# Kernel tuning notes

Hardware: AMD Instinct MI355X
Metric: run time of the kernel (lower is better)

The kernel has to match this reference:

```python
import jax, jax.numpy as jnp
import numpy as np

# --- quantization helpers (I-BERT-style symmetric quantization) ---

def _quant_int(x, scale, bit):
    # round(x/scale) clamped to signed `bit`-bit range (SymmetricQuantFunction)
    n = 2 ** (bit - 1) - 1
    return jnp.clip(jnp.round(x / scale), -n - 1, n)


def quant_linear(x, s_x, W, b, weight_bit=8):
    """QuantLinear: per-output-channel symmetric 8-bit weight quant, int GEMM, dequant.
    Returns (output, bias_scaling_factor[out_features])."""
    n = 2 ** (weight_bit - 1) - 1
    w_scale = jnp.maximum(jnp.max(jnp.abs(W), axis=1), 1e-8) / n          # (out,)
    w_int = _quant_int(W, w_scale[:, None], weight_bit)                   # int-valued (out,in)
    b_scale = w_scale * s_x                                               # (out,) broadcasts with scalar s_x
    b_int = jnp.round(b / b_scale)                                        # 32-bit bias, no clamp needed
    x_int = x / s_x                                                       # int-valued activations
    out_int = jnp.einsum('bsi,oi->bso', x_int, w_int) + b_int
    return out_int * b_scale, b_scale


def quant_act(x, bit):
    """QuantAct: per-tensor symmetric requantization to `bit` bits (dynamic min/max)."""
    n = 2 ** (bit - 1) - 1
    scale = jnp.maximum(jnp.max(jnp.abs(x)), 1e-8) / n                    # scalar
    x_int = _quant_int(x, scale, bit)
    return x_int * scale, scale


def int_gelu(x, s):
    """IntGELU (I-BERT): integer 2nd-order polynomial approximation of erf."""
    k = 1.4142
    c0, c1 = -0.2888, -1.769
    c2 = 1.0 / c0
    SHIFT = 14  # 'const' in the original code

    x_int = x / s
    se = s / k  # scaling factor fed to int_erf
    # --- int_erf ---
    b_int = jnp.floor(c1 / se)
    c_int = jnp.floor(c2 / se ** 2)
    sign = jnp.sign(x_int)
    abs_int = jnp.minimum(jnp.abs(x_int), -b_int)
    y_int = sign * ((abs_int + b_int) ** 2 + c_int)
    se2 = se ** 2 * c0
    y_int = jnp.floor(y_int / 2 ** SHIFT)
    se2 = se2 * 2 ** SHIFT
    # --- gelu = x * (erf/2 + 1/2) in integer form ---
    shift_int = jnp.floor(1.0 / se2)
    out_int = x_int * (y_int + shift_int)
    s_out = s * se2 / 2
    return out_int * s_out, s_out


def setup_inputs() -> dict:
    key = jax.random.key(0)
    k_x, k_w1, k_b1, k_w2, k_b2 = jax.random.split(key, 5)
    B, S, D, H = 8, 1024, 768, 3072
    x = jax.random.normal(k_x, (B, S, D), dtype=jnp.float32)
    act_scaling_factor = jnp.full((1,), 0.02, dtype=jnp.float32)
    # pre-quantize x onto its input grid (x arrives already quantized in the real pipeline)
    x = jnp.round(x / act_scaling_factor) * act_scaling_factor
    W1 = jax.random.normal(k_w1, (H, D), dtype=jnp.float32) * 0.02
    b1 = jax.random.normal(k_b1, (H,), dtype=jnp.float32) * 0.02
    W2 = jax.random.normal(k_w2, (D, H), dtype=jnp.float32) * 0.02
    b2 = jax.random.normal(k_b2, (D,), dtype=jnp.float32) * 0.02
    return {"x": x, "act_scaling_factor": act_scaling_factor,
            "W1": W1, "b1": b1, "W2": W2, "b2": b2}


def reference(x, act_scaling_factor, W1, b1, W2, b2):
    s = act_scaling_factor
    h, s = quant_linear(x, s, W1, b1)       # fc1: int8 GEMM + dequant
    h, s = quant_act(h, 8)                  # qact_gelu
    h, s = int_gelu(h, s)                   # IntGELU
    h, s = quant_act(h, 8)                  # qact1 (drop=0.0 -> identity)
    h, s = quant_linear(h, s, W2, b2)       # fc2
    h, s = quant_act(h, 16)                 # qact2 (16-bit)
    return h, s
```

## Files before the change

kernel.cpp:

```cpp
#include <hip/hip_runtime.h>

typedef _Float16 half8  __attribute__((ext_vector_type(8)));
typedef _Float16 half4v __attribute__((ext_vector_type(4)));
typedef float f32x4 __attribute__((ext_vector_type(4)));
typedef int int4v __attribute__((ext_vector_type(4)));

#define M_DIM 8192
#define D_DIM 768
#define H_DIM 3072

#define WS_WSCALE2   16
#define WS_BINT1     (WS_WSCALE2 + 768*4)
#define WS_BSCALE1   (WS_BINT1 + 3072*4)
#define WS_XQ        34560UL
#define WS_WQ1       (WS_XQ  + (size_t)M_DIM*D_DIM*2)
#define WS_WQ2I      (WS_WQ1 + (size_t)H_DIM*D_DIM*2)
#define WS_H1        (WS_WQ2I + (size_t)D_DIM*H_DIM)
#define WS_Q2        WS_H1
#define WS_H2        (WS_H1 + (size_t)M_DIM*H_DIM)
#define WS_Q1        (WS_H1 + (size_t)M_DIM*H_DIM*4)

__device__ __forceinline__ void gl_lds16(const _Float16* g, _Float16* l) {
  __builtin_amdgcn_global_load_lds(
      (const __attribute__((address_space(1))) void*)g,
      (__attribute__((address_space(3))) void*)l, 16, 0, 0);
}
__device__ __forceinline__ void gl_lds16c(const char* g, char* l) {
  __builtin_amdgcn_global_load_lds(
      (const __attribute__((address_space(1))) void*)g,
      (__attribute__((address_space(3))) void*)l, 16, 0, 0);
}
__device__ __forceinline__ void vmw4or0(bool four) {
  if (four) asm volatile("s_waitcnt vmcnt(4)" ::: "memory");
  else      asm volatile("s_waitcnt vmcnt(0)" ::: "memory");
}

struct GeluP { float scale1, bintg, cintg, shiftint, s_out; };

__device__ __forceinline__ GeluP gelu_params(float max1) {
  GeluP p;
  p.scale1 = fmaxf(max1, 1e-8f) / 127.0f;
  float se = p.scale1 / 1.4142f;
  p.bintg = floorf(-1.769f / se);
  p.cintg = floorf(((float)(1.0 / -0.2888)) / (se * se));
  float se2 = ((se * se) * -0.2888f) * 16384.0f;
  p.shiftint = floorf(1.0f / se2);
  p.s_out = (p.scale1 * se2) * 0.5f;
  return p;
}

__device__ __forceinline__ float gelu_val(const GeluP& p, float qf) {
  float sg = (qf > 0.f) ? 1.f : ((qf < 0.f) ? -1.f : 0.f);
  float aq = fminf(fabsf(qf), -p.bintg);
  float t = aq + p.bintg;
  float y = sg * (t * t + p.cintg);
  float yf = floorf(y * (1.0f / 16384.0f));
  return (qf * (yf + p.shiftint)) * p.s_out;
}

__global__ __launch_bounds__(256)
void k12_prep(const float* __restrict__ W1, const float* __restrict__ b1,
              const float* __restrict__ W2, const float* __restrict__ x,
              const float* __restrict__ sxp,
              _Float16* __restrict__ wq1, char* __restrict__ wq2i,
              float* __restrict__ wscale2, float* __restrict__ bint1,
              float* __restrict__ bscale1, _Float16* __restrict__ xq,
              unsigned* __restrict__ wsu)
{
  if (blockIdx.x == 0 && threadIdx.x == 0) { wsu[0] = 0u; wsu[1] = 0u; wsu[2] = 0u; }
  if (blockIdx.x < 960) {
    int w = blockIdx.x * 4 + (threadIdx.x >> 6);
    int lane = threadIdx.x & 63;
    if (w < H_DIM) {
      const float* row = W1 + (size_t)w * D_DIM;
      f32x4 v[3]; float m = 0.f;
#pragma unroll
      for (int t = 0; t < 3; t++) {
        v[t] = *(const f32x4*)(row + t * 256 + lane * 4);
#pragma unroll
        for (int j = 0; j < 4; j++) m = fmaxf(m, fabsf(v[t][j]));
      }
#pragma unroll
      for (int off = 32; off >= 1; off >>= 1) m = fmaxf(m, __shfl_xor(m, off));
      float wsc = fmaxf(m, 1e-8f) / 127.0f;
      _Float16* orow = wq1 + (size_t)w * D_DIM;
#pragma unroll
      for (int t = 0; t < 3; t++) {
        half4v h;
#pragma unroll
        for (int j = 0; j < 4; j++) {
          float q = fminf(fmaxf(rintf(v[t][j] / wsc), -128.f), 127.f);
          h[j] = (_Float16)q;
        }
        *(half4v*)(orow + t * 256 + lane * 4) = h;
      }
      if (lane == 0) {
        float bs = wsc * sxp[0];
        bint1[w] = rintf(b1[w] / bs);
        bscale1[w] = bs;
      }
    } else {
      int o = w - H_DIM;
      const float* row = W2 + (size_t)o * H_DIM;
      f32x4 v[12]; float m = 0.f;
#pragma unroll
      for (int t = 0; t < 12; t++) {
        v[t] = *(const f32x4*)(row + t * 256 + lane * 4);
#pragma unroll
        for (int j = 0; j < 4; j++) m = fmaxf(m, fabsf(v[t][j]));
      }
#pragma unroll
      for (int off = 32; off >= 1; off >>= 1) m = fmaxf(m, __shfl_xor(m, off));
      float wsc = fmaxf(m, 1e-8f) / 127.0f;
      unsigned* orow = (unsigned*)(wq2i + (size_t)o * H_DIM);
#pragma unroll
      for (int t = 0; t < 12; t++) {
        unsigned pk = 0;
#pragma unroll
        for (int j = 0; j < 4; j++) {
          float q = fminf(fmaxf(rintf(v[t][j] / wsc), -128.f), 127.f);
          pk |= ((unsigned)(unsigned char)(char)(int)q) << (8 * j);
        }
        orow[t * 64 + lane] = pk;
      }
      if (lane == 0) wscale2[o] = wsc;
    }
  } else {
    float sx = sxp[0];
    const int n4 = (M_DIM * D_DIM) / 4;
    const int stride = 1024 * 256;
    for (int i = (blockIdx.x - 960) * 256 + threadIdx.x; i < n4; i += stride) {
      f32x4 v = ((const f32x4*)x)[i];
      half4v h;
#pragma unroll
      for (int j = 0; j < 4; j++) h[j] = (_Float16)(v[j] / sx);
      ((half4v*)xq)[i] = h;
    }
  }
}

#define STAGE_A8(buf, h, t) do {                                              \
    const _Float16* _s = pa + (size_t)(h) * 128 * K + (size_t)(t) * 64;       \
    _Float16* _d = lds + (buf) * 32768 + (h) * 8192 + w * 512;                \
    gl_lds16(_s, _d);                                                         \
    gl_lds16(_s + (size_t)64 * K, _d + 4096);                                 \
  } while (0)
#define STAGE_B8(buf, h, t) do {                                              \
    const _Float16* _s = pb + (size_t)(h) * 128 * K + (size_t)(t) * 64;       \
    _Float16* _d = lds + (buf) * 32768 + 16384 + (h) * 8192 + w * 512;        \
    gl_lds16(_s, _d);                                                         \
    gl_lds16(_s + (size_t)64 * K, _d + 4096);                                 \
  } while (0)
#define PHASE8(buf, qq, DOB, STMT, VMSTMT) do {                               \
    const char* _sb = (const char*)lds + (buf) * 65536;                       \
    half8 a00 = *(const half8*)(_sb + abase + (2*(qq)) * 2048 + c0);          \
    half8 a01 = *(const half8*)(_sb + abase + (2*(qq)) * 2048 + c1);          \
    half8 a10 = *(const half8*)(_sb + abase + (2*(qq)+1) * 2048 + c0);        \
    half8 a11 = *(const half8*)(_sb + abase + (2*(qq)+1) * 2048 + c1);        \
    if (DOB) {                                                                \
      _Pragma("unroll")                                                       \
      for (int nf = 0; nf < 4; nf++) {                                        \
        bfr[nf][0] = *(const half8*)(_sb + bbase + nf * 2048 + c0);           \
        bfr[nf][1] = *(const half8*)(_sb + bbase + nf * 2048 + c1);           \
      }                                                                       \
    }                                                                         \
    STMT;                                                                     \
    VMSTMT;                                                                   \
    asm volatile("s_barrier" ::: "memory");                                   \
    __builtin_amdgcn_s_setprio(1);                                            \
    _Pragma("unroll")                                                         \
    for (int nf = 0; nf < 4; nf++) {                                          \
      acc[2*(qq)][nf]   = __builtin_amdgcn_mfma_f32_16x16x32_f16(a00, bfr[nf][0], acc[2*(qq)][nf],   0, 0, 0); \
      acc[2*(qq)][nf]   = __builtin_amdgcn_mfma_f32_16x16x32_f16(a01, bfr[nf][1], acc[2*(qq)][nf],   0, 0, 0); \
      acc[2*(qq)+1][nf] = __builtin_amdgcn_mfma_f32_16x16x32_f16(a10, bfr[nf][0], acc[2*(qq)+1][nf], 0, 0, 0); \
      acc[2*(qq)+1][nf] = __builtin_amdgcn_mfma_f32_16x16x32_f16(a11, bfr[nf][1], acc[2*(qq)+1][nf], 0, 0, 0); \
    }                                                                         \
    __builtin_amdgcn_s_setprio(0);                                            \
    asm volatile("s_barrier" ::: "memory");                                   \
  } while (0)

__global__ __launch_bounds__(512, 2)
void gemm_f16_8p(const _Float16* __restrict__ A, const _Float16* __restrict__ B,
                 const float* __restrict__ bint, const float* __restrict__ bscale,
                 float* __restrict__ C, unsigned* __restrict__ maxw, int N, int K)
{
  __shared__ _Float16 lds[65536];
  __shared__ float wred[8];
  const int tid = threadIdx.x;
  const int w = tid >> 6;
  const int l = tid & 63;
  const int m0 = blockIdx.x * 256;
  const int n0 = blockIdx.y * 256;
  const int wm = w >> 2;
  const int wn = w & 3;

  const int srow = 8 * w + (l >> 3);
  const int swc  = (l & 7) ^ (l >> 3);
  const _Float16* pa = A + (size_t)(m0 + srow) * K + swc * 8;
  const _Float16* pb = B + (size_t)(n0 + srow) * K + swc * 8;

  const int c0 = (((l >> 4)) ^ (l & 7)) * 16;
  const int c1 = ((4 + (l >> 4)) ^ (l & 7)) * 16;
  const int abase = (wm * 128 + (l & 15)) * 128;
  const int bbase = 32768 + (wn * 64 + (l & 15)) * 128;

  f32x4 acc[8][4];
#pragma unroll
  for (int i = 0; i < 8; i++)
#pragma unroll
    for (int j = 0; j < 4; j++) acc[i][j] = (f32x4){0.f, 0.f, 0.f, 0.f};
  half8 bfr[4][2];

  const int nt = K >> 6;
  STAGE_B8(0, 0, 0); STAGE_B8(0, 1, 0);
  STAGE_A8(0, 0, 0); STAGE_A8(0, 1, 0);
  STAGE_B8(1, 0, 1); STAGE_B8(1, 1, 1);
  asm volatile("s_waitcnt vmcnt(4)" ::: "memory");
  asm volatile("s_barrier" ::: "memory");

  for (int i = 0; i < (nt >> 1); ++i) {
    const int t0 = 2 * i, t1 = 2 * i + 1;
    const bool g = (t0 + 2 < nt);
    PHASE8(0, 0, true,  STAGE_A8(1, 0, t1), );
    PHASE8(0, 1, false, STAGE_A8(1, 1, t1), );
    PHASE8(0, 2, false, if (g) STAGE_B8(0, 0, t0 + 2), );
    PHASE8(0, 3, false, if (g) STAGE_B8(0, 1, t0 + 2), vmw4or0(g));
    PHASE8(1, 0, true,  if (g) STAGE_A8(0, 0, t0 + 2), );
    PHASE8(1, 1, false, if (g) STAGE_A8(0, 1, t0 + 2), );
    PHASE8(1, 2, false, if (g) STAGE_B8(1, 0, t1 + 2), );
    PHASE8(1, 3, false, if (g) STAGE_B8(1, 1, t1 + 2),
           if (g) asm volatile("s_waitcnt vmcnt(4)" ::: "memory"));
  }

  float tmax = 0.f;
  const int orow0 = m0 + wm * 128 + (l >> 4) * 4;
  const int ocol0 = n0 + wn * 64 + (l & 15);
#pragma unroll
  for (int nf = 0; nf < 4; nf++) {
    const int col = ocol0 + nf * 16;
    const float bi = bint[col];
    const float bs = bscale[col];
#pragma unroll
    for (int mi = 0; mi < 8; mi++) {
#pragma unroll
      for (int e = 0; e < 4; e++) {
        const int rowm = orow0 + mi * 16 + e;
        float v = (acc[mi][nf][e] + bi) * bs;
        C[(size_t)rowm * N + col] = v;
        tmax = fmaxf(tmax, fabsf(v));
      }
    }
  }
#pragma unroll
  for (int off = 32; off >= 1; off >>= 1) tmax = fmaxf(tmax, __shfl_xor(tmax, off));
  if (l == 0) wred[w] = tmax;
  __syncthreads();
  if (tid == 0) {
    float bm = 0.f;
#pragma unroll
    for (int i = 0; i < 8; i++) bm = fmaxf(bm, wred[i]);
    atomicMax(maxw, __float_as_uint(bm));
  }
}

__global__ __launch_bounds__(256)
void k4_gelu(const float* __restrict__ h1, const unsigned* __restrict__ wsu,
             char* __restrict__ q1, unsigned* __restrict__ maxw, int n4)
{
  GeluP p = gelu_params(__uint_as_float(wsu[0]));
  float tmax = 0.f;
  int stride = gridDim.x * blockDim.x;
  for (int i = blockIdx.x * blockDim.x + threadIdx.x; i < n4; i += stride) {
    f32x4 h = ((const f32x4*)h1)[i];
    unsigned pack = 0;
#pragma unroll
    for (int j = 0; j < 4; j++) {
      float qf = fminf(fmaxf(rintf(h[j] / p.scale1), -128.f), 127.f);
      tmax = fmaxf(tmax, fabsf(gelu_val(p, qf)));
      pack |= ((unsigned)(unsigned char)(char)(int)qf) << (8 * j);
    }
    ((unsigned*)q1)[i] = pack;
  }
#pragma unroll
  for (int off = 32; off >= 1; off >>= 1) tmax = fmaxf(tmax, __shfl_xor(tmax, off));
  __shared__ float wred[4];
  int wid = threadIdx.x >> 6;
  if ((threadIdx.x & 63) == 0) wred[wid] = tmax;
  __syncthreads();
  if (threadIdx.x == 0) {
    float bm = fmaxf(fmaxf(wred[0], wred[1]), fmaxf(wred[2], wred[3]));
    atomicMax(maxw, __float_as_uint(bm));
  }
}

__global__ __launch_bounds__(256)
void k5_q2(const char* __restrict__ q1, const unsigned* __restrict__ wsu,
           char* __restrict__ q2, int n16)
{
  GeluP p = gelu_params(__uint_as_float(wsu[0]));
  float scale2 = fmaxf(__uint_as_float(wsu[1]), 1e-8f) / 127.0f;
  int stride = gridDim.x * blockDim.x;
  for (int i = blockIdx.x * blockDim.x + threadIdx.x; i < n16; i += stride) {
    uint4 pk = ((const uint4*)q1)[i];
    uint4 o;
    unsigned* pw[4] = {&o.x, &o.y, &o.z, &o.w};
    unsigned pr[4] = {pk.x, pk.y, pk.z, pk.w};
#pragma unroll
    for (int w = 0; w < 4; w++) {
      unsigned acc = 0;
#pragma unroll
      for (int j = 0; j < 4; j++) {
        float qf = (float)(int)(signed char)(pr[w] >> (8 * j));
        float g = gelu_val(p, qf);
        float q2f = fminf(fmaxf(rintf(g / scale2), -128.f), 127.f);
        acc |= ((unsigned)(unsigned char)(char)(int)q2f) << (8 * j);
      }
      *pw[w] = acc;
    }
    ((uint4*)q2)[i] = o;
  }
}

#define I8_SLOT 12288

__global__ __launch_bounds__(256)
void gemm_i8_dp(const char* __restrict__ A, const char* __restrict__ B,
                const unsigned* __restrict__ wsu, const float* __restrict__ wscale2,
                const float* __restrict__ b2, float* __restrict__ C,
                unsigned* __restrict__ maxw, int N, int K)
{
  __shared__ char lds[3 * I8_SLOT];
  __shared__ float wred[4];
  const int tid = threadIdx.x;
  const int wid = tid >> 6;
  const int lane = tid & 63;
  const int m0 = blockIdx.x * 64;
  const int n0 = blockIdx.y * 128;
  const int wm = wid >> 1;
  const int wn = wid & 1;
  const float scale2 = fmaxf(__uint_as_float(wsu[1]), 1e-8f) / 127.0f;

  const int sr = tid >> 2;
  const int sc = tid & 3;
  const int csw = sc ^ ((sr >> 1) & 3);
  const char* pa  = A + (size_t)(m0 + sr) * K + csw * 16;
  const char* pb0 = B + (size_t)(n0 + sr) * K + csw * 16;
  const char* pb1 = B + (size_t)(n0 + 64 + sr) * K + csw * 16;

#define STAGE_I(t, s) do {                                                   \
    char* const base = lds + (s) * I8_SLOT + wid * 1024;                     \
    gl_lds16c(pa  + (size_t)(t) * 64, base);                                 \
    gl_lds16c(pb0 + (size_t)(t) * 64, base + 4096);                          \
    gl_lds16c(pb1 + (size_t)(t) * 64, base + 8192);                          \
  } while (0)

  int aoff[2], boff[4];
  const int ks = lane >> 4;
#pragma unroll
  for (int f = 0; f < 2; f++) {
    int r = wm * 32 + f * 16 + (lane & 15);
    aoff[f] = r * 64 + ((ks ^ ((r >> 1) & 3)) * 16);
  }
#pragma unroll
  for (int f = 0; f < 4; f++) {
    int rn = wn * 64 + f * 16 + (lane & 15);
    boff[f] = 4096 + rn * 64 + ((ks ^ ((rn >> 1) & 3)) * 16);
  }

  int4v acc[2][4];
#pragma unroll
  for (int i = 0; i < 2; i++)
#pragma unroll
    for (int j = 0; j < 4; j++) acc[i][j] = (int4v){0, 0, 0, 0};

  const int nt = K / 64;
  STAGE_I(0, 0);
  STAGE_I(1, 1);
  for (int t = 0; t < nt; ++t) {
    const int s = t % 3;
    if (t + 1 < nt) asm volatile("s_waitcnt vmcnt(3)" ::: "memory");
    else            asm volatile("s_waitcnt vmcnt(0)" ::: "memory");
    asm volatile("s_barrier" ::: "memory");
    if (t + 2 < nt) STAGE_I(t + 2, (t + 2) % 3);
    const char* sb = lds + s * I8_SLOT;
    int4v a[2], b01[2], b23[2];
#pragma unroll
    for (int f = 0; f < 2; f++) a[f] = *(const int4v*)(sb + aoff[f]);
    b01[0] = *(const int4v*)(sb + boff[0]);
    b01[1] = *(const int4v*)(sb + boff[1]);
    __builtin_amdgcn_s_setprio(1);
#pragma unroll
    for (int i = 0; i < 2; i++)
#pragma unroll
      for (int j = 0; j < 2; j++)
        acc[i][j] = __builtin_amdgcn_mfma_i32_16x16x64_i8(a[i], b01[j], acc[i][j], 0, 0, 0);
    __builtin_amdgcn_s_setprio(0);
    b23[0] = *(const int4v*)(sb + boff[2]);
    b23[1] = *(const int4v*)(sb + boff[3]);
    __builtin_amdgcn_s_setprio(1);
#pragma unroll
    for (int i = 0; i < 2; i++)
#pragma unroll
      for (int j = 0; j < 2; j++)
        acc[i][j + 2] = __builtin_amdgcn_mfma_i32_16x16x64_i8(a[i], b23[j], acc[i][j + 2], 0, 0, 0);
    __builtin_amdgcn_s_setprio(0);
  }
#undef STAGE_I

  float tmax = 0.f;
  const int orow0 = m0 + wm * 32 + (lane >> 4) * 4;
  const int ocol0 = n0 + wn * 64 + (lane & 15);
#pragma unroll
  for (int j = 0; j < 4; j++) {
    const int col = ocol0 + j * 16;
    const float bs = wscale2[col] * scale2;
    const float bi = rintf(b2[col] / bs);
#pragma unroll
    for (int i = 0; i < 2; i++) {
#pragma unroll
      for (int e = 0; e < 4; e++) {
        const int rowm = orow0 + i * 16 + e;
        float v = ((float)acc[i][j][e] + bi) * bs;
        C[(size_t)rowm * N + col] = v;
        tmax = fmaxf(tmax, fabsf(v));
      }
    }
  }
#pragma unroll
  for (int off = 32; off >= 1; off >>= 1) tmax = fmaxf(tmax, __shfl_xor(tmax, off));
  if (lane == 0) wred[wid] = tmax;
  __syncthreads();
  if (tid == 0) {
    float bm = fmaxf(fmaxf(wred[0], wred[1]), fmaxf(wred[2], wred[3]));
    atomicMax(maxw, __float_as_uint(bm));
  }
}

__global__ __launch_bounds__(256)
void k7_final(const float* __restrict__ h2, const unsigned* __restrict__ wsu,
              float* __restrict__ out, int n4, int ntot)
{
  float scale16 = fmaxf(__uint_as_float(wsu[2]), 1e-8f) / 32767.0f;
  int stride = gridDim.x * blockDim.x;
  for (int i = blockIdx.x * blockDim.x + threadIdx.x; i < n4; i += stride) {
    f32x4 v = ((const f32x4*)h2)[i];
    f32x4 o;
#pragma unroll
    for (int j = 0; j < 4; j++) {
      float q = fminf(fmaxf(rintf(v[j] / scale16), -32768.f), 32767.f);
      o[j] = q * scale16;
    }
    ((f32x4*)out)[i] = o;
  }
  if (blockIdx.x == 0 && threadIdx.x == 0) out[ntot] = scale16;
}

extern "C" void kernel_launch(void* const* d_in, const int* in_sizes, int n_in,
                              void* d_out, int out_size, void* d_ws, size_t ws_size,
                              hipStream_t stream)
{
  (void)in_sizes; (void)n_in; (void)out_size; (void)ws_size;
  const float* x  = (const float*)d_in[0];
  const float* sx = (const float*)d_in[1];
  const float* W1 = (const float*)d_in[2];
  const float* b1 = (const float*)d_in[3];
  const float* W2 = (const float*)d_in[4];
  const float* b2 = (const float*)d_in[5];
  float* out = (float*)d_out;
  char* ws = (char*)d_ws;

  unsigned* wsu   = (unsigned*)ws;
  float* wscale2  = (float*)(ws + WS_WSCALE2);
  float* bint1    = (float*)(ws + WS_BINT1);
  float* bscale1  = (float*)(ws + WS_BSCALE1);
  _Float16* xq    = (_Float16*)(ws + WS_XQ);
  _Float16* wq1   = (_Float16*)(ws + WS_WQ1);
  char* wq2i      = (char*)(ws + WS_WQ2I);
  float* h1       = (float*)(ws + WS_H1);
  char* q2        = (char*)(ws + WS_Q2);
  float* h2       = (float*)(ws + WS_H2);
  char* q1        = (char*)(ws + WS_Q1);

  k12_prep<<<dim3(1984), dim3(256), 0, stream>>>(W1, b1, W2, x, sx, wq1, wq2i,
                                                 wscale2, bint1, bscale1, xq, wsu);
  gemm_f16_8p<<<dim3(32, 12), dim3(512), 0, stream>>>(xq, wq1, bint1, bscale1, h1, wsu + 0, H_DIM, D_DIM);
  k4_gelu<<<dim3(2048), dim3(256), 0, stream>>>(h1, wsu, q1, wsu + 1, (M_DIM * H_DIM) / 4);
  k5_q2<<<dim3(2048), dim3(256), 0, stream>>>(q1, wsu, q2, (M_DIM * H_DIM) / 16);
  gemm_i8_dp<<<dim3(128, 6), dim3(256), 0, stream>>>(q2, wq2i, wsu, wscale2, b2, h2, wsu + 2, D_DIM, H_DIM);
  k7_final<<<dim3(2048), dim3(256), 0, stream>>>(h2, wsu, out, (M_DIM * D_DIM) / 4, M_DIM * D_DIM);
}
```

Baseline: 187.0 us.

## Rewrite fc1 f16 GEMM as 128x256 tile with triple-buffered K=32 pipeline

Replaces the 512-thread 256x256-tile fc1 GEMM, which used an 8-phase ping-pong schedule, with a 256-thread 128x256-tile kernel. The new kernel uses a simple three-slot LDS ring over K steps of 32 and one barrier per step. Each wave computes all 128 rows against its own 64 columns, so the grid doubles to 768 blocks for better CU balance. In exchange there are more barriers per unit of K, more A-fragment LDS reads per wave, and less B reuse per block.

```diff
diff --git a/kernel.cpp b/kernel.cpp
--- a/kernel.cpp
+++ b/kernel.cpp
@@ -30,10 +30,6 @@
       (const __attribute__((address_space(1))) void*)g,
       (__attribute__((address_space(3))) void*)l, 16, 0, 0);
 }
-__device__ __forceinline__ void vmw4or0(bool four) {
-  if (four) asm volatile("s_waitcnt vmcnt(4)" ::: "memory");
-  else      asm volatile("s_waitcnt vmcnt(0)" ::: "memory");
-}
 
 struct GeluP { float scale1, bintg, cintg, shiftint, s_out; };
 
@@ -139,113 +135,89 @@
   }
 }
 
-#define STAGE_A8(buf, h, t) do {                                              \
-    const _Float16* _s = pa + (size_t)(h) * 128 * K + (size_t)(t) * 64;       \
-    _Float16* _d = lds + (buf) * 32768 + (h) * 8192 + w * 512;                \
-    gl_lds16(_s, _d);                                                         \
-    gl_lds16(_s + (size_t)64 * K, _d + 4096);                                 \
-  } while (0)
-#define STAGE_B8(buf, h, t) do {                                              \
-    const _Float16* _s = pb + (size_t)(h) * 128 * K + (size_t)(t) * 64;       \
-    _Float16* _d = lds + (buf) * 32768 + 16384 + (h) * 8192 + w * 512;        \
-    gl_lds16(_s, _d);                                                         \
-    gl_lds16(_s + (size_t)64 * K, _d + 4096);                                 \
-  } while (0)
-#define PHASE8(buf, qq, DOB, STMT, VMSTMT) do {                               \
-    const char* _sb = (const char*)lds + (buf) * 65536;                       \
-    half8 a00 = *(const half8*)(_sb + abase + (2*(qq)) * 2048 + c0);          \
-    half8 a01 = *(const half8*)(_sb + abase + (2*(qq)) * 2048 + c1);          \
-    half8 a10 = *(const half8*)(_sb + abase + (2*(qq)+1) * 2048 + c0);        \
-    half8 a11 = *(const half8*)(_sb + abase + (2*(qq)+1) * 2048 + c1);        \
-    if (DOB) {                                                                \
-      _Pragma("unroll")                                                       \
-      for (int nf = 0; nf < 4; nf++) {                                        \
-        bfr[nf][0] = *(const half8*)(_sb + bbase + nf * 2048 + c0);           \
-        bfr[nf][1] = *(const half8*)(_sb + bbase + nf * 2048 + c1);           \
-      }                                                                       \
-    }                                                                         \
-    STMT;                                                                     \
-    VMSTMT;                                                                   \
-    asm volatile("s_barrier" ::: "memory");                                   \
-    __builtin_amdgcn_s_setprio(1);                                            \
-    _Pragma("unroll")                                                         \
-    for (int nf = 0; nf < 4; nf++) {                                          \
-      acc[2*(qq)][nf]   = __builtin_amdgcn_mfma_f32_16x16x32_f16(a00, bfr[nf][0], acc[2*(qq)][nf],   0, 0, 0); \
-      acc[2*(qq)][nf]   = __builtin_amdgcn_mfma_f32_16x16x32_f16(a01, bfr[nf][1], acc[2*(qq)][nf],   0, 0, 0); \
-      acc[2*(qq)+1][nf] = __builtin_amdgcn_mfma_f32_16x16x32_f16(a10, bfr[nf][0], acc[2*(qq)+1][nf], 0, 0, 0); \
-      acc[2*(qq)+1][nf] = __builtin_amdgcn_mfma_f32_16x16x32_f16(a11, bfr[nf][1], acc[2*(qq)+1][nf], 0, 0, 0); \
-    }                                                                         \
-    __builtin_amdgcn_s_setprio(0);                                            \
-    asm volatile("s_barrier" ::: "memory");                                   \
-  } while (0)
-
-__global__ __launch_bounds__(512, 2)
-void gemm_f16_8p(const _Float16* __restrict__ A, const _Float16* __restrict__ B,
+__global__ __launch_bounds__(256, 2)
+void gemm_f16_v8(const _Float16* __restrict__ A, const _Float16* __restrict__ B,
                  const float* __restrict__ bint, const float* __restrict__ bscale,
                  float* __restrict__ C, unsigned* __restrict__ maxw, int N, int K)
 {
-  __shared__ _Float16 lds[65536];
-  __shared__ float wred[8];
+  __shared__ _Float16 lds[3 * 12288];
+  __shared__ float wred[4];
   const int tid = threadIdx.x;
   const int w = tid >> 6;
   const int l = tid & 63;
-  const int m0 = blockIdx.x * 256;
+  const int m0 = blockIdx.x * 128;
   const int n0 = blockIdx.y * 256;
-  const int wm = w >> 2;
-  const int wn = w & 3;
-
-  const int srow = 8 * w + (l >> 3);
-  const int swc  = (l & 7) ^ (l >> 3);
-  const _Float16* pa = A + (size_t)(m0 + srow) * K + swc * 8;
-  const _Float16* pb = B + (size_t)(n0 + srow) * K + swc * 8;
-
-  const int c0 = (((l >> 4)) ^ (l & 7)) * 16;
-  const int c1 = ((4 + (l >> 4)) ^ (l & 7)) * 16;
-  const int abase = (wm * 128 + (l & 15)) * 128;
-  const int bbase = 32768 + (wn * 64 + (l & 15)) * 128;
+
+  const int sri = l >> 2;
+  const int csw = (l & 3) ^ ((l >> 3) & 3);
+  const _Float16* pag = A + (size_t)(m0 + 32 * w + sri) * K + csw * 8;
+  const _Float16* pbg = B + (size_t)(n0 + 64 * w + sri) * K + csw * 8;
+
+#define STAGE_F1(t, s) do {                                                   \
+    _Float16* const base = lds + (size_t)(s) * 12288;                         \
+    gl_lds16(pag + (size_t)(t) * 32,                   base + (2*w) * 512);   \
+    gl_lds16(pag + (size_t)16 * K + (size_t)(t) * 32,  base + (2*w+1) * 512); \
+    gl_lds16(pbg + (size_t)(t) * 32,                   base + 4096 + (4*w) * 512);   \
+    gl_lds16(pbg + (size_t)16 * K + (size_t)(t) * 32,  base + 4096 + (4*w+1) * 512); \
+    gl_lds16(pbg + (size_t)32 * K + (size_t)(t) * 32,  base + 4096 + (4*w+2) * 512); \
+    gl_lds16(pbg + (size_t)48 * K + (size_t)(t) * 32,  base + 4096 + (4*w+3) * 512); \
+  } while (0)
+
+  const int ks = l >> 4;
+  const int swc = ks ^ (((l & 15) >> 1) & 3);
+  int abyte[8], bbyte[4];
+#pragma unroll
+  for (int fa = 0; fa < 8; fa++)
+    abyte[fa] = (fa * 16 + (l & 15)) * 64 + swc * 16;
+#pragma unroll
+  for (int fb = 0; fb < 4; fb++)
+    bbyte[fb] = 8192 + (w * 64 + fb * 16 + (l & 15)) * 64 + swc * 16;
 
   f32x4 acc[8][4];
 #pragma unroll
   for (int i = 0; i < 8; i++)
 #pragma unroll
     for (int j = 0; j < 4; j++) acc[i][j] = (f32x4){0.f, 0.f, 0.f, 0.f};
-  half8 bfr[4][2];
-
-  const int nt = K >> 6;
-  STAGE_B8(0, 0, 0); STAGE_B8(0, 1, 0);
-  STAGE_A8(0, 0, 0); STAGE_A8(0, 1, 0);
-  STAGE_B8(1, 0, 1); STAGE_B8(1, 1, 1);
-  asm volatile("s_waitcnt vmcnt(4)" ::: "memory");
-  asm volatile("s_barrier" ::: "memory");
-
-  for (int i = 0; i < (nt >> 1); ++i) {
-    const int t0 = 2 * i, t1 = 2 * i + 1;
-    const bool g = (t0 + 2 < nt);
-    PHASE8(0, 0, true,  STAGE_A8(1, 0, t1), );
-    PHASE8(0, 1, false, STAGE_A8(1, 1, t1), );
-    PHASE8(0, 2, false, if (g) STAGE_B8(0, 0, t0 + 2), );
-    PHASE8(0, 3, false, if (g) STAGE_B8(0, 1, t0 + 2), vmw4or0(g));
-    PHASE8(1, 0, true,  if (g) STAGE_A8(0, 0, t0 + 2), );
-    PHASE8(1, 1, false, if (g) STAGE_A8(0, 1, t0 + 2), );
-    PHASE8(1, 2, false, if (g) STAGE_B8(1, 0, t1 + 2), );
-    PHASE8(1, 3, false, if (g) STAGE_B8(1, 1, t1 + 2),
-           if (g) asm volatile("s_waitcnt vmcnt(4)" ::: "memory"));
-  }
+
+  const int nt = K / 32;
+  STAGE_F1(0, 0);
+  STAGE_F1(1, 1);
+  for (int t = 0; t < nt; ++t) {
+    const int s = t % 3;
+    if (t + 1 < nt) asm volatile("s_waitcnt vmcnt(6)" ::: "memory");
+    else            asm volatile("s_waitcnt vmcnt(0)" ::: "memory");
+    asm volatile("s_barrier" ::: "memory");
+    if (t + 2 < nt) STAGE_F1(t + 2, (t + 2) % 3);
+    const char* sb = (const char*)(lds + (size_t)s * 12288);
+    half8 a[8], b[4];
+#pragma unroll
+    for (int fa = 0; fa < 8; fa++) a[fa] = *(const half8*)(sb + abyte[fa]);
+#pragma unroll
+    for (int fb = 0; fb < 4; fb++) b[fb] = *(const half8*)(sb + bbyte[fb]);
+    __builtin_amdgcn_s_setprio(1);
+#pragma unroll
+    for (int fa = 0; fa < 8; fa++)
+#pragma unroll
+      for (int fb = 0; fb < 4; fb++)
+        acc[fa][fb] = __builtin_amdgcn_mfma_f32_16x16x32_f16(a[fa], b[fb], acc[fa][fb], 0, 0, 0);
+    __builtin_amdgcn_s_setprio(0);
+  }
+#undef STAGE_F1
 
   float tmax = 0.f;
-  const int orow0 = m0 + wm * 128 + (l >> 4) * 4;
-  const int ocol0 = n0 + wn * 64 + (l & 15);
-#pragma unroll
-  for (int nf = 0; nf < 4; nf++) {
-    const int col = ocol0 + nf * 16;
+  const int orow0 = m0 + (l >> 4) * 4;
+  const int ocol0 = n0 + w * 64 + (l & 15);
+#pragma unroll
+  for (int fb = 0; fb < 4; fb++) {
+    const int col = ocol0 + fb * 16;
     const float bi = bint[col];
     const float bs = bscale[col];
 #pragma unroll
-    for (int mi = 0; mi < 8; mi++) {
+    for (int fa = 0; fa < 8; fa++) {
 #pragma unroll
       for (int e = 0; e < 4; e++) {
-        const int rowm = orow0 + mi * 16 + e;
-        float v = (acc[mi][nf][e] + bi) * bs;
+        const int rowm = orow0 + fa * 16 + e;
+        float v = (acc[fa][fb][e] + bi) * bs;
         C[(size_t)rowm * N + col] = v;
         tmax = fmaxf(tmax, fabsf(v));
       }
@@ -256,9 +228,7 @@
   if (l == 0) wred[w] = tmax;
   __syncthreads();
   if (tid == 0) {
-    float bm = 0.f;
-#pragma unroll
-    for (int i = 0; i < 8; i++) bm = fmaxf(bm, wred[i]);
+    float bm = fmaxf(fmaxf(wred[0], wred[1]), fmaxf(wred[2], wred[3]));
     atomicMax(maxw, __float_as_uint(bm));
   }
 }
@@ -348,7 +318,7 @@
   const char* pb1 = B + (size_t)(n0 + 64 + sr) * K + csw * 16;
 
 #define STAGE_I(t, s) do {                                                   \
-    char* const base = lds + (s) * I8_SLOT + wid * 1024;                     \
+    char* const base = lds + (size_t)(s) * I8_SLOT + wid * 1024;             \
     gl_lds16c(pa  + (size_t)(t) * 64, base);                                 \
     gl_lds16c(pb0 + (size_t)(t) * 64, base + 4096);                          \
     gl_lds16c(pb1 + (size_t)(t) * 64, base + 8192);                          \
@@ -382,7 +352,7 @@
     else            asm volatile("s_waitcnt vmcnt(0)" ::: "memory");
     asm volatile("s_barrier" ::: "memory");
     if (t + 2 < nt) STAGE_I(t + 2, (t + 2) % 3);
-    const char* sb = lds + s * I8_SLOT;
+    const char* sb = lds + (size_t)s * I8_SLOT;
     int4v a[2], b01[2], b23[2];
 #pragma unroll
     for (int f = 0; f < 2; f++) a[f] = *(const int4v*)(sb + aoff[f]);
@@ -483,7 +453,7 @@
 
   k12_prep<<<dim3(1984), dim3(256), 0, stream>>>(W1, b1, W2, x, sx, wq1, wq2i,
                                                  wscale2, bint1, bscale1, xq, wsu);
-  gemm_f16_8p<<<dim3(32, 12), dim3(512), 0, stream>>>(xq, wq1, bint1, bscale1, h1, wsu + 0, H_DIM, D_DIM);
+  gemm_f16_v8<<<dim3(64, 12), dim3(256), 0, stream>>>(xq, wq1, bint1, bscale1, h1, wsu + 0, H_DIM, D_DIM);
   k4_gelu<<<dim3(2048), dim3(256), 0, stream>>>(h1, wsu, q1, wsu + 1, (M_DIM * H_DIM) / 4);
   k5_q2<<<dim3(2048), dim3(256), 0, stream>>>(q1, wsu, q2, (M_DIM * H_DIM) / 16);
   gemm_i8_dp<<<dim3(128, 6), dim3(256), 0, stream>>>(q2, wq2i, wsu, wscale2, b2, h2, wsu + 2, D_DIM, H_DIM);
```

New measurement: 187.5 us. Within noise of the previous version (+0.3%).
